# Kernel tuning notes

Measured on AMD Instinct MI355X. Metric: run time of the kernel, lower is better.

## Reference

```python
import jax, jax.numpy as jnp
import numpy as np

N, F, R, E, L = 100000, 128, 4, 1600000, 2


def setup_inputs() -> dict:
    key = jax.random.key(0)
    k1, k2, k3, k4, k5 = jax.random.split(key, 5)
    scale = 1.0 / np.sqrt(F)
    x = jax.random.normal(k1, (N, F), dtype=jnp.float32)
    edge_index = jax.random.randint(k2, (2, E), 0, N, dtype=jnp.int64)
    edge_type = jax.random.randint(k3, (E,), 0, R, dtype=jnp.int64)
    weights = jax.random.normal(k4, (L, R, F, F), dtype=jnp.float32) * scale
    roots = jax.random.normal(k5, (L, F, F), dtype=jnp.float32) * scale
    biases = jnp.zeros((L, F), dtype=jnp.float32)
    return {"x": x, "edge_index": edge_index, "edge_type": edge_type,
            "weights": weights, "roots": roots, "biases": biases}


def _rgcn_layer(x, weight, root, bias, src, dst, etype):
    # weight: [R, F, F]. Transform all nodes by all relation weights: [R, N, F]
    xw = jnp.einsum('nf,rfo->rno', x, weight)
    msgs = xw[etype, src]                       # [E, F] gather per edge
    seg = dst * R + etype                       # combined (node, relation) segment id
    sums = jax.ops.segment_sum(msgs, seg, num_segments=N * R)
    cnt = jax.ops.segment_sum(jnp.ones((msgs.shape[0],), msgs.dtype), seg,
                              num_segments=N * R)
    mean = sums / jnp.maximum(cnt, 1.0)[:, None]  # mean aggregation per relation
    agg = mean.reshape(N, R, F).sum(axis=1)       # sum over relations: [N, F]
    return agg + x @ root + bias


def reference(x, edge_index, edge_type, weights, roots, biases):
    src, dst = edge_index[0], edge_index[1]
    for l in range(L):
        x = _rgcn_layer(x, weights[l], roots[l], biases[l], src, dst, edge_type)
        x = jax.nn.relu(x)  # dropout is identity at eval
    return x
```

## Files before the change

kernel.cpp:

```cpp
#include <hip/hip_runtime.h>
#include <hip/hip_bf16.h>

#define N_NODES 100000
#define FDIM 128
#define RREL 4
#define NEDGE 1600000
#define NSEG (N_NODES * RREL)
#define KB_TOT 20
#define BSW_PER_LAYER (KB_TOT * 8 * 64 * 8)
#define BIN_SHIFT 10
#define BIN_SEGS 1024
#define NBINS ((NSEG + BIN_SEGS - 1) / BIN_SEGS)
#define BIN_CAP 5120
#define EPB 2048
#define CAST_NB ((N_NODES * FDIM / 4) / 256)
#define PREP_NB (2 * BSW_PER_LAYER / 256)

typedef __attribute__((ext_vector_type(8))) short bfrag;
typedef __attribute__((ext_vector_type(4))) float ffrag;

__device__ __forceinline__ unsigned short f2bf(float f) {
    unsigned u = __float_as_uint(f);
    u += 0x7fffu + ((u >> 16) & 1u);
    return (unsigned short)(u >> 16);
}
__device__ __forceinline__ float bf_lo(unsigned u) { return __uint_as_float(u << 16); }
__device__ __forceinline__ float bf_hi(unsigned u) { return __uint_as_float(u & 0xffff0000u); }

__global__ __launch_bounds__(256) void prep(
    const float* __restrict__ x, unsigned short* __restrict__ xb,
    const float* __restrict__ W,
    const float* __restrict__ root,
    unsigned short* __restrict__ Bsw,
    int* __restrict__ binCursor)
{
    if (blockIdx.x < CAST_NB) {
        int i = blockIdx.x * 256 + threadIdx.x;
        float4 v = ((const float4*)x)[i];
        ushort4 o = { f2bf(v.x), f2bf(v.y), f2bf(v.z), f2bf(v.w) };
        ((ushort4*)xb)[i] = o;
        return;
    }
    int wb = blockIdx.x - CAST_NB;
    int idx = wb * 256 + threadIdx.x;
    if (wb < 2) {
        int t = wb * 256 + threadIdx.x;
        if (t < NBINS) binCursor[t] = 0;
    }
    int layer = idx / BSW_PER_LAYER;
    int rem = idx % BSW_PER_LAYER;
    int kb = rem / 4096;
    int rem2 = rem % 4096;
    int ct = rem2 / 512;
    int rem3 = rem2 % 512;
    int lane = rem3 / 8;
    int j = rem3 % 8;
    int k = kb * 32 + (lane >> 4) * 8 + j;
    int n = ct * 16 + (lane & 15);
    float v;
    if (k < 512) v = W[(size_t)layer * 4 * 128 * 128 + (size_t)k * 128 + n];
    else         v = root[(size_t)layer * 128 * 128 + (size_t)(k - 512) * 128 + n];
    Bsw[idx] = f2bf(v);
}

__global__ __launch_bounds__(256) void bin_scatter(
    const int* __restrict__ src, const int* __restrict__ dst,
    const int* __restrict__ et, int* __restrict__ binCursor,
    unsigned* __restrict__ pairs)
{
    __shared__ int hist[NBINS];
    __shared__ int base[NBINS];
    int tid = threadIdx.x;
    for (int b = tid; b < NBINS; b += 256) hist[b] = 0;
    __syncthreads();
    int e0 = blockIdx.x * EPB;
    int binr[EPB / 256];
    unsigned pkr[EPB / 256];
    #pragma unroll
    for (int i = 0; i < EPB / 256; ++i) {
        int e = e0 + i * 256 + tid;
        if (e < NEDGE) {
            int seg = dst[e] * RREL + et[e];
            binr[i] = seg >> BIN_SHIFT;
            pkr[i] = ((unsigned)src[e] << BIN_SHIFT) | (unsigned)(seg & (BIN_SEGS - 1));
            atomicAdd(&hist[binr[i]], 1);
        } else binr[i] = -1;
    }
    __syncthreads();
    for (int b = tid; b < NBINS; b += 256) {
        int h = hist[b];
        base[b] = h ? atomicAdd(&binCursor[b], h) : 0;
        hist[b] = 0;
    }
    __syncthreads();
    #pragma unroll
    for (int i = 0; i < EPB / 256; ++i) {
        if (binr[i] >= 0) {
            int b = binr[i];
            int li = atomicAdd(&hist[b], 1);
            pairs[(size_t)b * BIN_CAP + base[b] + li] = pkr[i];
        }
    }
}

__global__ __launch_bounds__(1024) void bin_fill(
    const unsigned* __restrict__ pairs, const int* __restrict__ binCursor,
    int* __restrict__ esrc, int* __restrict__ counts, int* __restrict__ cursor)
{
    __shared__ int hist[BIN_SEGS];
    __shared__ int cur[BIN_SEGS];
    __shared__ int waveSums[16];
    int b = blockIdx.x;
    int tid = threadIdx.x;
    int seg0 = b << BIN_SHIFT;
    int cnt = binCursor[b];
    size_t pb = (size_t)b * BIN_CAP;
    hist[tid] = 0;
    __syncthreads();
    for (int i = tid; i < cnt; i += 1024)
        atomicAdd(&hist[pairs[pb + i] & (BIN_SEGS - 1)], 1);
    __syncthreads();
    int v = hist[tid];
    int lane = tid & 63, wv = tid >> 6;
    int inc = v;
    #pragma unroll
    for (int d = 1; d < 64; d <<= 1) {
        int o = __shfl_up(inc, d, 64);
        if (lane >= d) inc += o;
    }
    if (lane == 63) waveSums[wv] = inc;
    __syncthreads();
    int wbase = 0;
    for (int w = 0; w < wv; ++w) wbase += waveSums[w];
    int glob = (int)pb + wbase + inc - v;
    int sg = seg0 + tid;
    if (sg < NSEG) { counts[sg] = v; cursor[sg] = glob; }
    cur[tid] = glob;
    __syncthreads();
    for (int i = tid; i < cnt; i += 1024) {
        unsigned p = pairs[pb + i];
        int pos = atomicAdd(&cur[p & (BIN_SEGS - 1)], 1);
        esrc[pos] = (int)(p >> BIN_SHIFT);
    }
}

__device__ __forceinline__ uint4 ldrow(const unsigned short* xb, int s, int lane16) {
    unsigned off = (unsigned)s * (FDIM * 2) + (unsigned)lane16 * 16u;
    return *(const uint4*)((const char*)xb + off);
}
__device__ __forceinline__ void acc_add(float* acc, uint4 u) {
    acc[0] += bf_lo(u.x); acc[1] += bf_hi(u.x);
    acc[2] += bf_lo(u.y); acc[3] += bf_hi(u.y);
    acc[4] += bf_lo(u.z); acc[5] += bf_hi(u.z);
    acc[6] += bf_lo(u.w); acc[7] += bf_hi(u.w);
}

__global__ __launch_bounds__(256) void rgcn_aggregate(
    const unsigned short* __restrict__ xb, const int* __restrict__ esrc,
    const int* __restrict__ cursor, const int* __restrict__ counts,
    unsigned short* __restrict__ meanb)
{
    int sub = threadIdx.x >> 4;
    int lane16 = threadIdx.x & 15;
    int seg = blockIdx.x * 16 + sub;
    int j = cursor[seg];
    int c = counts[seg];
    int end = j + c;
    float acc[8] = {};
    for (; j + 3 < end; j += 4) {
        int s0 = esrc[j], s1 = esrc[j + 1], s2 = esrc[j + 2], s3 = esrc[j + 3];
        uint4 u0 = ldrow(xb, s0, lane16);
        uint4 u1 = ldrow(xb, s1, lane16);
        uint4 u2 = ldrow(xb, s2, lane16);
        uint4 u3 = ldrow(xb, s3, lane16);
        acc_add(acc, u0); acc_add(acc, u1); acc_add(acc, u2); acc_add(acc, u3);
    }
    for (; j < end; ++j) {
        int sv = esrc[j];
        uint4 u = ldrow(xb, sv, lane16);
        acc_add(acc, u);
    }
    float inv = 1.0f / fmaxf((float)c, 1.0f);
    uint4 o;
    o.x = (unsigned)f2bf(acc[0] * inv) | ((unsigned)f2bf(acc[1] * inv) << 16);
    o.y = (unsigned)f2bf(acc[2] * inv) | ((unsigned)f2bf(acc[3] * inv) << 16);
    o.z = (unsigned)f2bf(acc[4] * inv) | ((unsigned)f2bf(acc[5] * inv) << 16);
    o.w = (unsigned)f2bf(acc[6] * inv) | ((unsigned)f2bf(acc[7] * inv) << 16);
    ((uint4*)(meanb + (size_t)seg * FDIM))[lane16] = o;
}

__global__ __launch_bounds__(256, 2) void rgcn_transform(
    const unsigned short* __restrict__ xb,
    const unsigned short* __restrict__ meanb,
    const unsigned short* __restrict__ Bsw,
    const float* __restrict__ bias,
    float* __restrict__ out,
    unsigned short* __restrict__ xbn,
    const int writeF32)
{
    int tid = threadIdx.x;
    int wave = tid >> 6, lane = tid & 63;
    int quad = lane >> 4, rlo = lane & 15;
    int n0 = blockIdx.x * 128 + wave * 32;
    int r0c = min(n0 + rlo, N_NODES - 1);
    int r1c = min(n0 + 16 + rlo, N_NODES - 1);

    const bfrag* m0 = (const bfrag*)(meanb + (size_t)r0c * 512) + quad;
    const bfrag* m1 = (const bfrag*)(meanb + (size_t)r1c * 512) + quad;
    const bfrag* x0 = (const bfrag*)(xb + (size_t)r0c * FDIM) + quad;
    const bfrag* x1 = (const bfrag*)(xb + (size_t)r1c * FDIM) + quad;
    const bfrag* bl = (const bfrag*)Bsw + lane;

    ffrag acc[2][8] = {};

    #pragma unroll 2
    for (int kb = 0; kb < 16; ++kb) {
        bfrag a0 = m0[kb * 4];
        bfrag a1 = m1[kb * 4];
        #pragma unroll
        for (int ct = 0; ct < 8; ++ct) {
            bfrag b = bl[(kb * 8 + ct) * 64];
            acc[0][ct] = __builtin_amdgcn_mfma_f32_16x16x32_bf16(a0, b, acc[0][ct], 0, 0, 0);
            acc[1][ct] = __builtin_amdgcn_mfma_f32_16x16x32_bf16(a1, b, acc[1][ct], 0, 0, 0);
        }
    }
    #pragma unroll 2
    for (int kb = 16; kb < 20; ++kb) {
        bfrag a0 = x0[(kb - 16) * 4];
        bfrag a1 = x1[(kb - 16) * 4];
        #pragma unroll
        for (int ct = 0; ct < 8; ++ct) {
            bfrag b = bl[(kb * 8 + ct) * 64];
            acc[0][ct] = __builtin_amdgcn_mfma_f32_16x16x32_bf16(a0, b, acc[0][ct], 0, 0, 0);
            acc[1][ct] = __builtin_amdgcn_mfma_f32_16x16x32_bf16(a1, b, acc[1][ct], 0, 0, 0);
        }
    }

    float bcol[8];
    #pragma unroll
    for (int ct = 0; ct < 8; ++ct) bcol[ct] = bias[ct * 16 + rlo];

    #pragma unroll
    for (int rt = 0; rt < 2; ++rt) {
        int rbase = n0 + rt * 16 + quad * 4;
        #pragma unroll
        for (int i = 0; i < 4; ++i) {
            int r = rbase + i;
            if (r < N_NODES) {
                #pragma unroll
                for (int ct = 0; ct < 8; ++ct) {
                    float v = fmaxf(acc[rt][ct][i] + bcol[ct], 0.0f);
                    int col = ct * 16 + rlo;
                    if (writeF32) out[(size_t)r * FDIM + col] = v;
                    else          xbn[(size_t)r * FDIM + col] = f2bf(v);
                }
            }
        }
    }
}

extern "C" void kernel_launch(void* const* d_in, const int* in_sizes, int n_in,
                              void* d_out, int out_size, void* d_ws, size_t ws_size,
                              hipStream_t stream) {
    const float* x        = (const float*)d_in[0];
    const int* edge_index = (const int*)d_in[1];
    const int* edge_type  = (const int*)d_in[2];
    const float* weights  = (const float*)d_in[3];
    const float* roots    = (const float*)d_in[4];
    const float* biases   = (const float*)d_in[5];
    float* out = (float*)d_out;

    unsigned short* meanb = (unsigned short*)d_ws;
    unsigned* pairs = (unsigned*)d_ws;
    unsigned short* xb0   = meanb + (size_t)NSEG * FDIM;
    unsigned short* xb1   = xb0 + (size_t)N_NODES * FDIM;
    unsigned short* Bsw   = xb1 + (size_t)N_NODES * FDIM;
    int* esrc   = (int*)(Bsw + 2 * BSW_PER_LAYER);
    int* counts = esrc + (size_t)NBINS * BIN_CAP;
    int* cursor = counts + NSEG;
    int* binCursor = cursor + NSEG;

    const int* src = edge_index;
    const int* dst = edge_index + NEDGE;

    prep<<<CAST_NB + PREP_NB, 256, 0, stream>>>(x, xb0, weights, roots, Bsw,
                                                binCursor);
    bin_scatter<<<(NEDGE + EPB - 1) / EPB, 256, 0, stream>>>(src, dst, edge_type,
                                                             binCursor, pairs);
    bin_fill<<<NBINS, 1024, 0, stream>>>(pairs, binCursor, esrc, counts, cursor);

    const int tgrid = (N_NODES + 127) / 128;

    rgcn_aggregate<<<NSEG / 16, 256, 0, stream>>>(xb0, esrc, cursor, counts, meanb);
    rgcn_transform<<<tgrid, 256, 0, stream>>>(xb0, meanb, Bsw, biases, out, xb1, 0);
    rgcn_aggregate<<<NSEG / 16, 256, 0, stream>>>(xb1, esrc, cursor, counts, meanb);
    rgcn_transform<<<tgrid, 256, 0, stream>>>(xb1, meanb, Bsw + BSW_PER_LAYER,
                                              biases + FDIM, out, xb0, 1);
}
```

Before: 392.6 us.

## Stage B weight tiles through double-buffered LDS and prefetch A fragments

The transform kernel now copies each k-block of the swizzled weight matrix into a double-buffered shared-memory tile, shared by all four waves, instead of every wave reading it from global memory. A fragments are prefetched two k-blocks ahead in registers. The two k-loops are merged into one fully unrolled loop with a barrier per step, and the occupancy hint goes from 2 to 3 blocks. The per-step __syncthreads and the added register pressure from prefetching could limit overlap.

```diff
diff --git a/kernel.cpp b/kernel.cpp
--- a/kernel.cpp
+++ b/kernel.cpp
@@ -189,7 +189,7 @@
     ((uint4*)(meanb + (size_t)seg * FDIM))[lane16] = o;
 }
 
-__global__ __launch_bounds__(256, 2) void rgcn_transform(
+__global__ __launch_bounds__(256, 3) void rgcn_transform(
     const unsigned short* __restrict__ xb,
     const unsigned short* __restrict__ meanb,
     const unsigned short* __restrict__ Bsw,
@@ -198,43 +198,63 @@
     unsigned short* __restrict__ xbn,
     const int writeF32)
 {
+    __shared__ __align__(16) unsigned char Bsm[2][8192];
+
     int tid = threadIdx.x;
     int wave = tid >> 6, lane = tid & 63;
     int quad = lane >> 4, rlo = lane & 15;
     int n0 = blockIdx.x * 128 + wave * 32;
-    int r0c = min(n0 + rlo, N_NODES - 1);
-    int r1c = min(n0 + 16 + rlo, N_NODES - 1);
+    int r0 = n0 + rlo;
+    int r1 = n0 + 16 + rlo;
+    int r0c = min(r0, N_NODES - 1);
+    int r1c = min(r1, N_NODES - 1);
 
     const bfrag* m0 = (const bfrag*)(meanb + (size_t)r0c * 512) + quad;
     const bfrag* m1 = (const bfrag*)(meanb + (size_t)r1c * 512) + quad;
     const bfrag* x0 = (const bfrag*)(xb + (size_t)r0c * FDIM) + quad;
     const bfrag* x1 = (const bfrag*)(xb + (size_t)r1c * FDIM) + quad;
-    const bfrag* bl = (const bfrag*)Bsw + lane;
+
+    const uint4* gB = (const uint4*)Bsw;
+    #define STAGE_B(kb, buf) do { \
+        uint4* _s = (uint4*)Bsm[buf]; \
+        const uint4* _g = gB + (kb) * 512; \
+        _s[tid] = _g[tid]; \
+        _s[tid + 256] = _g[tid + 256]; \
+    } while (0)
+
+    #define AFRAG(row, kb) ((kb) < 16 ? row##_m[(kb) * 4] : row##_x[((kb) - 16) * 4])
+    const bfrag* r0_m = m0; const bfrag* r0_x = x0;
+    const bfrag* r1_m = m1; const bfrag* r1_x = x1;
 
     ffrag acc[2][8] = {};
 
-    #pragma unroll 2
-    for (int kb = 0; kb < 16; ++kb) {
-        bfrag a0 = m0[kb * 4];
-        bfrag a1 = m1[kb * 4];
+    STAGE_B(0, 0);
+    bfrag a0p0 = AFRAG(r0, 0), a1p0 = AFRAG(r1, 0);
+    bfrag a0p1 = AFRAG(r0, 1), a1p1 = AFRAG(r1, 1);
+    __syncthreads();
+
+    #pragma unroll
+    for (int kb = 0; kb < KB_TOT; ++kb) {
+        int cur = kb & 1;
+        if (kb + 1 < KB_TOT) STAGE_B(kb + 1, cur ^ 1);
+
+        bfrag a0 = cur ? a0p1 : a0p0;
+        bfrag a1 = cur ? a1p1 : a1p0;
+        if (kb + 2 < KB_TOT) {
+            if (cur) { a0p1 = AFRAG(r0, kb + 2); a1p1 = AFRAG(r1, kb + 2); }
+            else     { a0p0 = AFRAG(r0, kb + 2); a1p0 = AFRAG(r1, kb + 2); }
+        }
+
         #pragma unroll
         for (int ct = 0; ct < 8; ++ct) {
-            bfrag b = bl[(kb * 8 + ct) * 64];
+            bfrag b = *(const bfrag*)&Bsm[cur][ct * 1024 + lane * 16];
             acc[0][ct] = __builtin_amdgcn_mfma_f32_16x16x32_bf16(a0, b, acc[0][ct], 0, 0, 0);
             acc[1][ct] = __builtin_amdgcn_mfma_f32_16x16x32_bf16(a1, b, acc[1][ct], 0, 0, 0);
         }
-    }
-    #pragma unroll 2
-    for (int kb = 16; kb < 20; ++kb) {
-        bfrag a0 = x0[(kb - 16) * 4];
-        bfrag a1 = x1[(kb - 16) * 4];
-        #pragma unroll
-        for (int ct = 0; ct < 8; ++ct) {
-            bfrag b = bl[(kb * 8 + ct) * 64];
-            acc[0][ct] = __builtin_amdgcn_mfma_f32_16x16x32_bf16(a0, b, acc[0][ct], 0, 0, 0);
-            acc[1][ct] = __builtin_amdgcn_mfma_f32_16x16x32_bf16(a1, b, acc[1][ct], 0, 0, 0);
-        }
-    }
+        __syncthreads();
+    }
+    #undef STAGE_B
+    #undef AFRAG
 
     float bcol[8];
     #pragma unroll
```

Result: faster. 368.6 us (-6.1%).
